# Optimization experiments

Measured on AMD Instinct MI355X. Metric: run time of the kernel, lower is better.

Reference implementation:

```python
import jax, jax.numpy as jnp
import numpy as np

B, M, Q, D = 32, 8192, 64, 128

def setup_inputs() -> dict:
    key = jax.random.key(0)
    k1, k2, k3, k4 = jax.random.split(key, 4)
    story_a = jax.random.normal(k1, (B, M, D), dtype=jnp.float32)
    u = jax.random.normal(k2, (B, Q, D), dtype=jnp.float32)
    story_c = jax.random.normal(k3, (B, M, D), dtype=jnp.float32)
    H = jax.random.normal(k4, (D, D), dtype=jnp.float32) * (1.0 / np.sqrt(D))
    return {"story_a": story_a, "u": u, "story_c": story_c, "H": H}

def reference(story_a, u, story_c, H):
    # scores: Dot(axes=-1)([story_a, u]) -> (B, M, Q)
    m = jnp.einsum('bmd,bqd->bmq', story_a, u)
    # Keras Softmax() default axis=-1: normalize over Q (faithful to original)
    p = jax.nn.softmax(m, axis=-1)          # (B, M, Q)
    p = jnp.swapaxes(p, 1, 2)                # (B, Q, M)
    # output memory: Dot(axes=(2,1))([p, story_c]) -> (B, Q, D)
    c = jnp.einsum('bqm,bmd->bqd', p, story_c)
    # linear residual: K.dot(u, H) + c
    mapped_u = jnp.einsum('bqd,de->bqe', u, H)
    return c + mapped_u
```

## Files before the change

kernel.cpp:

```cpp
#include <hip/hip_runtime.h>

#define B_ 32
#define M_ 8192
#define Q_ 64
#define D_ 128
#define MT 64
#define CHN 16
#define NT (M_ / (CHN * MT))
#define LDP 72
#define LDU 136

typedef __attribute__((ext_vector_type(8))) short short8;
typedef __attribute__((ext_vector_type(4))) float floatx4;

__device__ __forceinline__ unsigned pkbf(float a, float b) {
  unsigned ua = __builtin_bit_cast(unsigned, a) + 0x8000u;
  unsigned ub = __builtin_bit_cast(unsigned, b) + 0x8000u;
  return __builtin_amdgcn_perm(ub, ua, 0x07060302u);
}

__device__ __forceinline__ short8 pack8(float4 a, float4 b) {
  union { unsigned u[4]; short8 v; } o;
  o.u[0] = pkbf(a.x, a.y); o.u[1] = pkbf(a.z, a.w);
  o.u[2] = pkbf(b.x, b.y); o.u[3] = pkbf(b.z, b.w);
  return o.v;
}

template <int CTRL>
__device__ __forceinline__ float dppadd(float x) {
  int y = __builtin_amdgcn_update_dpp(0, __builtin_bit_cast(int, x), CTRL, 0xF, 0xF, true);
  return x + __builtin_bit_cast(float, y);
}
__device__ __forceinline__ float rowsum16(float x) {
  x = dppadd<0x128>(x); x = dppadd<0x124>(x);
  x = dppadd<0x122>(x); x = dppadd<0x121>(x);
  return x;
}

__device__ __forceinline__ void barrier_lds() {
  asm volatile("s_waitcnt lgkmcnt(0)\n\ts_barrier" ::: "memory");
}

template <bool ATOMIC>
__global__ __launch_bounds__(256, 2) void memn2n_main(
    const float* __restrict__ A, const float* __restrict__ U,
    const float* __restrict__ Cc, float* __restrict__ dst) {
  __shared__ __align__(16) unsigned short sU[Q_ * LDU];
  __shared__ __align__(16) unsigned short sP[2][Q_ * LDP];

  const int tid  = threadIdx.x;
  const int lane = tid & 63;
  const int w    = tid >> 6;
  const int l15  = lane & 15;
  const int quad = (lane >> 4) & 3;

  const int blk = blockIdx.x;
  const int b   = blk / CHN;
  const int ch  = blk - b * CHN;

  const float* Abase = A + ((size_t)b * M_ + (size_t)ch * NT * MT) * D_;
  const float* Cbase = Cc + ((size_t)b * M_ + (size_t)ch * NT * MT) * D_;

  {
    const float* ub = U + (size_t)b * Q_ * D_;
#pragma unroll
    for (int i = 0; i < 8; ++i) {
      int idx = tid + i * 256;
      int q = idx >> 5, c4 = idx & 31;
      float4 v = *(const float4*)(ub + q * D_ + c4 * 4);
      *(uint2*)&sU[q * LDU + c4 * 4] = make_uint2(pkbf(v.x, v.y), pkbf(v.z, v.w));
    }
  }

  const float* Ap = Abase + ((size_t)(16 * w + l15) * D_ + 8 * quad);
  const float* Cp = Cbase + (size_t)(8 * quad) * D_ + 32 * w + l15;

  float4 a_st[8];
  float  c_st[32];

#pragma unroll
  for (int ks = 0; ks < 4; ++ks) {
    a_st[2 * ks]     = *(const float4*)(Ap + 32 * ks);
    a_st[2 * ks + 1] = *(const float4*)(Ap + 32 * ks + 4);
  }
#pragma unroll
  for (int ks = 0; ks < 2; ++ks)
#pragma unroll
    for (int ds = 0; ds < 2; ++ds)
#pragma unroll
      for (int j = 0; j < 8; ++j)
        c_st[(2 * ks + ds) * 8 + j] = Cp[(size_t)(32 * ks + j) * D_ + 16 * ds];

  barrier_lds();

  floatx4 acc[2][4];
#pragma unroll
  for (int i = 0; i < 2; ++i)
#pragma unroll
    for (int j = 0; j < 4; ++j) acc[i][j] = (floatx4){0.f, 0.f, 0.f, 0.f};

  for (int t = 0; t < NT; ++t) {
    short8 af[4];
#pragma unroll
    for (int ks = 0; ks < 4; ++ks) af[ks] = pack8(a_st[2 * ks], a_st[2 * ks + 1]);

    if (t + 1 < NT) {
      const float* An = Ap + (size_t)(t + 1) * MT * D_;
#pragma unroll
      for (int ks = 0; ks < 4; ++ks) {
        a_st[2 * ks]     = *(const float4*)(An + 32 * ks);
        a_st[2 * ks + 1] = *(const float4*)(An + 32 * ks + 4);
      }
    }

    floatx4 s1[4];
#pragma unroll
    for (int qs = 0; qs < 4; ++qs) s1[qs] = (floatx4){0.f, 0.f, 0.f, 0.f};
#pragma unroll
    for (int ks = 0; ks < 4; ++ks)
#pragma unroll
      for (int qs = 0; qs < 4; ++qs) {
        short8 uq = *(const short8*)&sU[(16 * qs + l15) * LDU + 32 * ks + 8 * quad];
        s1[qs] = __builtin_amdgcn_mfma_f32_16x16x32_bf16(af[ks], uq, s1[qs], 0, 0, 0);
      }

    float pv[4][4];
#pragma unroll
    for (int rg = 0; rg < 4; ++rg) {
      const float c = 1.4426950408889634f;
      float e0 = exp2f(s1[0][rg] * c), e1 = exp2f(s1[1][rg] * c);
      float e2 = exp2f(s1[2][rg] * c), e3 = exp2f(s1[3][rg] * c);
      float sm = (e0 + e1) + (e2 + e3);
      sm = rowsum16(sm);
      float inv = __builtin_amdgcn_rcpf(sm);
      pv[0][rg] = e0 * inv; pv[1][rg] = e1 * inv;
      pv[2][rg] = e2 * inv; pv[3][rg] = e3 * inv;
    }

    unsigned short* sPt = &sP[t & 1][0];
#pragma unroll
    for (int qs = 0; qs < 4; ++qs)
      *(uint2*)&sPt[(16 * qs + l15) * LDP + 16 * w + 4 * quad] =
          make_uint2(pkbf(pv[qs][0], pv[qs][1]), pkbf(pv[qs][2], pv[qs][3]));

    barrier_lds();

    short8 cf[4];
#pragma unroll
    for (int ks = 0; ks < 2; ++ks)
#pragma unroll
      for (int ds = 0; ds < 2; ++ds) {
        const float* cc = &c_st[(2 * ks + ds) * 8];
        union { unsigned u[4]; short8 v; } o;
        o.u[0] = pkbf(cc[0], cc[1]); o.u[1] = pkbf(cc[2], cc[3]);
        o.u[2] = pkbf(cc[4], cc[5]); o.u[3] = pkbf(cc[6], cc[7]);
        cf[2 * ks + ds] = o.v;
      }

    if (t + 1 < NT) {
      const float* Cn = Cp + (size_t)(t + 1) * MT * D_;
#pragma unroll
      for (int ks = 0; ks < 2; ++ks)
#pragma unroll
        for (int ds = 0; ds < 2; ++ds)
#pragma unroll
          for (int j = 0; j < 8; ++j)
            c_st[(2 * ks + ds) * 8 + j] = Cn[(size_t)(32 * ks + j) * D_ + 16 * ds];
    }

#pragma unroll
    for (int ks = 0; ks < 2; ++ks) {
      short8 pa[4];
#pragma unroll
      for (int qs = 0; qs < 4; ++qs)
        pa[qs] = *(const short8*)&sPt[(16 * qs + l15) * LDP + 32 * ks + 8 * quad];
#pragma unroll
      for (int ds = 0; ds < 2; ++ds)
#pragma unroll
        for (int qs = 0; qs < 4; ++qs)
          acc[ds][qs] =
              __builtin_amdgcn_mfma_f32_16x16x32_bf16(pa[qs], cf[2 * ks + ds], acc[ds][qs], 0, 0, 0);
    }
  }

  if (ATOMIC) {
#pragma unroll
    for (int ds = 0; ds < 2; ++ds)
#pragma unroll
      for (int qs = 0; qs < 4; ++qs)
#pragma unroll
        for (int rg = 0; rg < 4; ++rg) {
          int q = qs * 16 + quad * 4 + rg;
          int d = l15 + 16 * (2 * w + ds);
          atomicAdd(&dst[((size_t)b * Q_ + q) * D_ + d], acc[ds][qs][rg]);
        }
  } else {
    float* pp = dst + (((size_t)ch * B_ + b) * Q_) * D_;
#pragma unroll
    for (int ds = 0; ds < 2; ++ds)
#pragma unroll
      for (int qs = 0; qs < 4; ++qs)
#pragma unroll
        for (int rg = 0; rg < 4; ++rg) {
          int q = qs * 16 + quad * 4 + rg;
          int d = l15 + 16 * (2 * w + ds);
          pp[q * D_ + d] = acc[ds][qs][rg];
        }
  }
}

__global__ __launch_bounds__(128) void memn2n_reduce(
    const float* __restrict__ U, const float* __restrict__ H,
    const float* __restrict__ part, float* __restrict__ out, int chunks) {
  int bq = blockIdx.x;
  int b = bq >> 6, q = bq & 63;
  int d = threadIdx.x;
  __shared__ float su[D_];
  size_t row = ((size_t)b * Q_ + q) * D_;
  su[d] = U[row + d];
  __syncthreads();
  float acc = 0.f;
#pragma unroll 16
  for (int e = 0; e < D_; ++e) acc = fmaf(su[e], H[e * D_ + d], acc);
#pragma unroll 8
  for (int ch = 0; ch < chunks; ++ch)
    acc += part[(((size_t)ch * B_ + b) * Q_ + q) * D_ + d];
  out[row + d] = acc;
}

extern "C" void kernel_launch(void* const* d_in, const int* in_sizes, int n_in,
                              void* d_out, int out_size, void* d_ws, size_t ws_size,
                              hipStream_t stream) {
  const float* A  = (const float*)d_in[0];
  const float* U  = (const float*)d_in[1];
  const float* Cc = (const float*)d_in[2];
  const float* H  = (const float*)d_in[3];
  float* out = (float*)d_out;

  size_t part_bytes = (size_t)CHN * B_ * Q_ * D_ * sizeof(float);
  if (ws_size >= part_bytes) {
    float* part = (float*)d_ws;
    memn2n_main<false><<<B_ * CHN, 256, 0, stream>>>(A, U, Cc, part);
    memn2n_reduce<<<B_ * Q_, 128, 0, stream>>>(U, H, part, out, CHN);
  } else {
    memn2n_reduce<<<B_ * Q_, 128, 0, stream>>>(U, H, nullptr, out, 0);
    memn2n_main<true><<<B_ * CHN, 256, 0, stream>>>(A, U, Cc, out);
  }
}
```

Measured before the change: 291.6 us.

## Stage A and C tiles through per-wave LDS with coalesced nontemporal float4 loads

Global loads of A and C change from per-lane strided reads (scalar C loads spanning many rows) to coalesced float4 rows, issued as nontemporal loads. Each wave writes the rows into its own padded LDS scratch and reads them back in MFMA fragment layout. The aim is to raise effective HBM bandwidth on this streaming, memory-bound kernel. In exchange it adds LDS traffic, extra wave-local write/read ordering, and more LDS per block, which could reduce occupancy.

```diff
diff --git a/kernel.cpp b/kernel.cpp
--- a/kernel.cpp
+++ b/kernel.cpp
@@ -9,6 +9,7 @@
 #define NT (M_ / (CHN * MT))
 #define LDP 72
 #define LDU 136
+#define SAP 36
 
 typedef __attribute__((ext_vector_type(8))) short short8;
 typedef __attribute__((ext_vector_type(4))) float floatx4;
@@ -24,6 +25,11 @@
   o.u[0] = pkbf(a.x, a.y); o.u[1] = pkbf(a.z, a.w);
   o.u[2] = pkbf(b.x, b.y); o.u[3] = pkbf(b.z, b.w);
   return o.v;
+}
+
+__device__ __forceinline__ float4 nt4(const float* p) {
+  floatx4 v = __builtin_nontemporal_load((const floatx4*)p);
+  return make_float4(v[0], v[1], v[2], v[3]);
 }
 
 template <int CTRL>
@@ -47,12 +53,16 @@
     const float* __restrict__ Cc, float* __restrict__ dst) {
   __shared__ __align__(16) unsigned short sU[Q_ * LDU];
   __shared__ __align__(16) unsigned short sP[2][Q_ * LDP];
+  __shared__ __align__(16) float sA[4][16 * SAP];
+  __shared__ __align__(16) float sC[4][32 * SAP];
 
   const int tid  = threadIdx.x;
   const int lane = tid & 63;
   const int w    = tid >> 6;
   const int l15  = lane & 15;
   const int quad = (lane >> 4) & 3;
+  const int lr   = lane >> 3;
+  const int lc   = lane & 7;
 
   const int blk = blockIdx.x;
   const int b   = blk / CHN;
@@ -60,6 +70,20 @@
 
   const float* Abase = A + ((size_t)b * M_ + (size_t)ch * NT * MT) * D_;
   const float* Cbase = Cc + ((size_t)b * M_ + (size_t)ch * NT * MT) * D_;
+
+  const float* ApL = Abase + ((size_t)(16 * w + lr) * D_) + 4 * lc;
+  const float* CpL = Cbase + ((size_t)lr * D_) + 32 * w + 4 * lc;
+
+  float4 aR[8];
+  float4 cR[8];
+
+#pragma unroll
+  for (int ks = 0; ks < 4; ++ks) {
+    aR[2 * ks]     = nt4(ApL + 32 * ks);
+    aR[2 * ks + 1] = nt4(ApL + 32 * ks + 8 * (size_t)D_);
+  }
+#pragma unroll
+  for (int g = 0; g < 8; ++g) cR[g] = nt4(CpL + (size_t)(8 * g) * D_);
 
   {
     const float* ub = U + (size_t)b * Q_ * D_;
@@ -72,27 +96,11 @@
     }
   }
 
-  const float* Ap = Abase + ((size_t)(16 * w + l15) * D_ + 8 * quad);
-  const float* Cp = Cbase + (size_t)(8 * quad) * D_ + 32 * w + l15;
-
-  float4 a_st[8];
-  float  c_st[32];
-
-#pragma unroll
-  for (int ks = 0; ks < 4; ++ks) {
-    a_st[2 * ks]     = *(const float4*)(Ap + 32 * ks);
-    a_st[2 * ks + 1] = *(const float4*)(Ap + 32 * ks + 4);
-  }
-#pragma unroll
-  for (int ks = 0; ks < 2; ++ks)
-#pragma unroll
-    for (int ds = 0; ds < 2; ++ds)
-#pragma unroll
-      for (int j = 0; j < 8; ++j)
-        c_st[(2 * ks + ds) * 8 + j] = Cp[(size_t)(32 * ks + j) * D_ + 16 * ds];
-
   barrier_lds();
 
+  float* const sAw = sA[w];
+  float* const sCw = sC[w];
+
   floatx4 acc[2][4];
 #pragma unroll
   for (int i = 0; i < 2; ++i)
@@ -100,29 +108,27 @@
     for (int j = 0; j < 4; ++j) acc[i][j] = (floatx4){0.f, 0.f, 0.f, 0.f};
 
   for (int t = 0; t < NT; ++t) {
-    short8 af[4];
-#pragma unroll
-    for (int ks = 0; ks < 4; ++ks) af[ks] = pack8(a_st[2 * ks], a_st[2 * ks + 1]);
-
-    if (t + 1 < NT) {
-      const float* An = Ap + (size_t)(t + 1) * MT * D_;
-#pragma unroll
-      for (int ks = 0; ks < 4; ++ks) {
-        a_st[2 * ks]     = *(const float4*)(An + 32 * ks);
-        a_st[2 * ks + 1] = *(const float4*)(An + 32 * ks + 4);
-      }
-    }
-
     floatx4 s1[4];
 #pragma unroll
     for (int qs = 0; qs < 4; ++qs) s1[qs] = (floatx4){0.f, 0.f, 0.f, 0.f};
 #pragma unroll
-    for (int ks = 0; ks < 4; ++ks)
+    for (int ks = 0; ks < 4; ++ks) {
+      *(float4*)&sAw[(0 + lr) * SAP + 4 * lc] = aR[2 * ks];
+      *(float4*)&sAw[(8 + lr) * SAP + 4 * lc] = aR[2 * ks + 1];
+      if (t + 1 < NT) {
+        const float* An = ApL + (size_t)(t + 1) * MT * D_;
+        aR[2 * ks]     = nt4(An + 32 * ks);
+        aR[2 * ks + 1] = nt4(An + 32 * ks + 8 * (size_t)D_);
+      }
+      float4 x = *(const float4*)&sAw[l15 * SAP + 8 * quad];
+      float4 y = *(const float4*)&sAw[l15 * SAP + 8 * quad + 4];
+      short8 af = pack8(x, y);
 #pragma unroll
       for (int qs = 0; qs < 4; ++qs) {
         short8 uq = *(const short8*)&sU[(16 * qs + l15) * LDU + 32 * ks + 8 * quad];
-        s1[qs] = __builtin_amdgcn_mfma_f32_16x16x32_bf16(af[ks], uq, s1[qs], 0, 0, 0);
-      }
+        s1[qs] = __builtin_amdgcn_mfma_f32_16x16x32_bf16(af, uq, s1[qs], 0, 0, 0);
+      }
+    }
 
     float pv[4][4];
 #pragma unroll
@@ -143,43 +149,46 @@
       *(uint2*)&sPt[(16 * qs + l15) * LDP + 16 * w + 4 * quad] =
           make_uint2(pkbf(pv[qs][0], pv[qs][1]), pkbf(pv[qs][2], pv[qs][3]));
 
+#pragma unroll
+    for (int g = 0; g < 4; ++g)
+      *(float4*)&sCw[(8 * g + lr) * SAP + 4 * lc] = cR[g];
+    if (t + 1 < NT) {
+      const float* Cn = CpL + (size_t)(t + 1) * MT * D_;
+#pragma unroll
+      for (int g = 0; g < 4; ++g) cR[g] = nt4(Cn + (size_t)(8 * g) * D_);
+    }
+
     barrier_lds();
 
-    short8 cf[4];
-#pragma unroll
-    for (int ks = 0; ks < 2; ++ks)
+#pragma unroll
+    for (int ks = 0; ks < 2; ++ks) {
+      if (ks == 1) {
+#pragma unroll
+        for (int g = 4; g < 8; ++g)
+          *(float4*)&sCw[(8 * (g - 4) + lr) * SAP + 4 * lc] = cR[g];
+        if (t + 1 < NT) {
+          const float* Cn = CpL + (size_t)(t + 1) * MT * D_;
+#pragma unroll
+          for (int g = 4; g < 8; ++g) cR[g] = nt4(Cn + (size_t)(8 * g) * D_);
+        }
+      }
+      short8 pa[4];
+#pragma unroll
+      for (int qs = 0; qs < 4; ++qs)
+        pa[qs] = *(const short8*)&sPt[(16 * qs + l15) * LDP + 32 * ks + 8 * quad];
 #pragma unroll
       for (int ds = 0; ds < 2; ++ds) {
-        const float* cc = &c_st[(2 * ks + ds) * 8];
+        float cc[8];
+#pragma unroll
+        for (int j = 0; j < 8; ++j)
+          cc[j] = sCw[(8 * quad + j) * SAP + 16 * ds + l15];
         union { unsigned u[4]; short8 v; } o;
         o.u[0] = pkbf(cc[0], cc[1]); o.u[1] = pkbf(cc[2], cc[3]);
         o.u[2] = pkbf(cc[4], cc[5]); o.u[3] = pkbf(cc[6], cc[7]);
-        cf[2 * ks + ds] = o.v;
-      }
-
-    if (t + 1 < NT) {
-      const float* Cn = Cp + (size_t)(t + 1) * MT * D_;
-#pragma unroll
-      for (int ks = 0; ks < 2; ++ks)
-#pragma unroll
-        for (int ds = 0; ds < 2; ++ds)
-#pragma unroll
-          for (int j = 0; j < 8; ++j)
-            c_st[(2 * ks + ds) * 8 + j] = Cn[(size_t)(32 * ks + j) * D_ + 16 * ds];
-    }
-
-#pragma unroll
-    for (int ks = 0; ks < 2; ++ks) {
-      short8 pa[4];
-#pragma unroll
-      for (int qs = 0; qs < 4; ++qs)
-        pa[qs] = *(const short8*)&sPt[(16 * qs + l15) * LDP + 32 * ks + 8 * quad];
-#pragma unroll
-      for (int ds = 0; ds < 2; ++ds)
 #pragma unroll
         for (int qs = 0; qs < 4; ++qs)
-          acc[ds][qs] =
-              __builtin_amdgcn_mfma_f32_16x16x32_bf16(pa[qs], cf[2 * ks + ds], acc[ds][qs], 0, 0, 0);
+          acc[ds][qs] = __builtin_amdgcn_mfma_f32_16x16x32_bf16(pa[qs], o.v, acc[ds][qs], 0, 0, 0);
+      }
     }
   }
 
```

Measured after the change: 266.4 us. 8.6% less time.
